# Optimization experiments

Hardware: AMD Instinct MI355X
Metric: run time of the kernel (lower is better)

The kernel has to match this reference:

```python
import jax, jax.numpy as jnp
import numpy as np

B, L, D = 2, 2048, 1024
H, NL = 16, 8
DH = D // H  # 64


def setup_inputs() -> dict:
    key = jax.random.key(0)
    ks = jax.random.split(key, 16)
    s_d = 1.0 / np.sqrt(D)
    s_ff = 1.0 / np.sqrt(4 * D)
    f32 = jnp.float32
    return {
        "x": jax.random.normal(ks[0], (B, L, D), f32),
        "pe": jax.random.normal(ks[1], (L, D), f32) / 10.0,
        "wq": jax.random.normal(ks[2], (NL, D, D), f32) * s_d,
        "wk": jax.random.normal(ks[3], (NL, D, D), f32) * s_d,
        "wv": jax.random.normal(ks[4], (NL, D, D), f32) * s_d,
        "ln1_g": 1.0 + 0.02 * jax.random.normal(ks[5], (NL, D), f32),
        "ln1_b": 0.02 * jax.random.normal(ks[6], (NL, D), f32),
        "w1": jax.random.normal(ks[7], (NL, D, 4 * D), f32) * s_d,
        "b1": jax.random.normal(ks[8], (NL, 4 * D), f32) * s_d,
        "w2": jax.random.normal(ks[9], (NL, 4 * D, D), f32) * s_ff,
        "b2": jax.random.normal(ks[10], (NL, D), f32) * s_ff,
        "ln2_g": 1.0 + 0.02 * jax.random.normal(ks[11], (NL, D), f32),
        "ln2_b": 0.02 * jax.random.normal(ks[12], (NL, D), f32),
    }


def _layernorm(x, g, b, eps=1e-5):
    m = jnp.mean(x, axis=-1, keepdims=True)
    v = jnp.mean(jnp.square(x - m), axis=-1, keepdims=True)
    return (x - m) * jax.lax.rsqrt(v + eps) * g + b


def reference(x, pe, wq, wk, wv, ln1_g, ln1_b, w1, b1, w2, b2, ln2_g, ln2_b):
    Bb, T, Dd = x.shape
    h = x + pe[:T]
    causal = jnp.tril(jnp.ones((T, T), dtype=bool))  # [T,T]
    inv_sqrt_dh = np.float32(1.0 / np.sqrt(DH))

    def step(h, p):
        wq_, wk_, wv_, g1, be1, w1_, bb1, w2_, bb2, g2, be2 = p
        # QKV: [B,T,D] -> [B,H,T,DH]
        q = (h @ wq_).reshape(Bb, T, H, DH).transpose(0, 2, 1, 3)
        k = (h @ wk_).reshape(Bb, T, H, DH).transpose(0, 2, 1, 3)
        v = (h @ wv_).reshape(Bb, T, H, DH).transpose(0, 2, 1, 3)
        scores = jnp.einsum('bhqd,bhkd->bhqk', q, k)
        scores = jnp.where(causal, scores, -jnp.inf)
        attn = jax.nn.softmax(scores * inv_sqrt_dh, axis=-1)
        o = jnp.einsum('bhqk,bhkd->bhqd', attn, v)
        o = o.transpose(0, 2, 1, 3).reshape(Bb, T, Dd)
        h = _layernorm(h + o, g1, be1)
        mlp = jax.nn.selu(h @ w1_ + bb1) @ w2_ + bb2
        h = _layernorm(h + mlp, g2, be2)
        return h, None

    h, _ = jax.lax.scan(step, h, (wq, wk, wv, ln1_g, ln1_b, w1, b1, w2, b2, ln2_g, ln2_b))
    return h
```

## Files before the change

kernel.cpp:

```cpp
#include <hip/hip_runtime.h>
#include <stdint.h>

typedef unsigned short u16;
typedef __bf16 bf16x8 __attribute__((ext_vector_type(8)));
typedef __bf16 bf16x4 __attribute__((ext_vector_type(4)));
typedef float f32x4 __attribute__((ext_vector_type(4)));

__device__ __forceinline__ float b2f(u16 b) {
    return __builtin_bit_cast(float, ((unsigned)b) << 16);
}
__device__ __forceinline__ u16 f2b(float f) {
    unsigned u = __builtin_bit_cast(unsigned, f);
    return (u16)((u + 0x7fffu + ((u >> 16) & 1u)) >> 16);
}
__device__ __forceinline__ void async16(const void* g, void* l) {
    __builtin_amdgcn_global_load_lds((const __attribute__((address_space(1))) void*)g,
                                     (__attribute__((address_space(3))) void*)l, 16, 0, 0);
}

__global__ __launch_bounds__(256) void add_pe_kernel(const float* __restrict__ x,
                                                     const float* __restrict__ pe,
                                                     float* __restrict__ hf,
                                                     u16* __restrict__ hb) {
    const size_t i = ((size_t)blockIdx.x * 256 + threadIdx.x) * 4;
    float4 xv = *(const float4*)(x + i);
    float4 pv = *(const float4*)(pe + (i & 2097151));
    float4 f;
    f.x = xv.x + pv.x; f.y = xv.y + pv.y; f.z = xv.z + pv.z; f.w = xv.w + pv.w;
    *(float4*)(hf + i) = f;
    ushort4 hv;
    hv.x = f2b(f.x); hv.y = f2b(f.y); hv.z = f2b(f.z); hv.w = f2b(f.w);
    *(ushort4*)(hb + i) = hv;
}

__global__ __launch_bounds__(256) void transpose_cast_kernel(const float* __restrict__ src,
                                                             u16* __restrict__ dst,
                                                             int srcStride, int K) {
    __shared__ __align__(16) u16 tile[64 * 72];
    const int n0 = blockIdx.x * 64, k0 = blockIdx.y * 64;
    const int t = threadIdx.x;
    const int r = t >> 3, c8 = (t & 7) * 8;
#pragma unroll
    for (int ph = 0; ph < 2; ph++) {
        const int rr = r + ph * 32;
        const float* s = src + (size_t)(k0 + rr) * srcStride + n0 + c8;
        float4 a = *(const float4*)s;
        float4 b = *(const float4*)(s + 4);
        u16* tr = tile + rr * 72 + c8;
        tr[0] = f2b(a.x); tr[1] = f2b(a.y); tr[2] = f2b(a.z); tr[3] = f2b(a.w);
        tr[4] = f2b(b.x); tr[5] = f2b(b.y); tr[6] = f2b(b.z); tr[7] = f2b(b.w);
    }
    __syncthreads();
#pragma unroll
    for (int ph = 0; ph < 2; ph++) {
        const int rr = r + ph * 32;
        union { float4 f; u16 u[8]; } ov;
#pragma unroll
        for (int j = 0; j < 8; j++) ov.u[j] = tile[(c8 + j) * 72 + rr];
        *(float4*)(dst + (size_t)(n0 + rr) * K + k0 + c8) = ov.f;
    }
}

__global__ __launch_bounds__(256) void transpose_qkv_kernel(const float* __restrict__ wq,
                                                            const float* __restrict__ wk,
                                                            const float* __restrict__ wv,
                                                            u16* __restrict__ dst) {
    __shared__ __align__(16) u16 tile[64 * 72];
    const float* src = (blockIdx.z == 0) ? wq : (blockIdx.z == 1) ? wk : wv;
    u16* d = dst + (size_t)blockIdx.z * 1048576;
    const int n0 = blockIdx.x * 64, k0 = blockIdx.y * 64;
    const int t = threadIdx.x;
    const int r = t >> 3, c8 = (t & 7) * 8;
#pragma unroll
    for (int ph = 0; ph < 2; ph++) {
        const int rr = r + ph * 32;
        const float* s = src + (size_t)(k0 + rr) * 1024 + n0 + c8;
        float4 a = *(const float4*)s;
        float4 b = *(const float4*)(s + 4);
        u16* tr = tile + rr * 72 + c8;
        tr[0] = f2b(a.x); tr[1] = f2b(a.y); tr[2] = f2b(a.z); tr[3] = f2b(a.w);
        tr[4] = f2b(b.x); tr[5] = f2b(b.y); tr[6] = f2b(b.z); tr[7] = f2b(b.w);
    }
    __syncthreads();
#pragma unroll
    for (int ph = 0; ph < 2; ph++) {
        const int rr = r + ph * 32;
        union { float4 f; u16 u[8]; } ov;
#pragma unroll
        for (int j = 0; j < 8; j++) ov.u[j] = tile[(c8 + j) * 72 + rr];
        *(float4*)(d + (size_t)(n0 + rr) * 1024 + k0 + c8) = ov.f;
    }
}

__global__ __launch_bounds__(256) void transpose_v_kernel(const u16* __restrict__ src,
                                                          u16* __restrict__ dst) {
    __shared__ __align__(16) u16 tile[64 * 72];
    const int bh = blockIdx.y, t0 = blockIdx.x * 64;
    const int t = threadIdx.x;
    const int r = t >> 3, c8 = (t & 7) * 8;
    const size_t base = (size_t)bh * 131072;
#pragma unroll
    for (int ph = 0; ph < 2; ph++) {
        const int rr = r + ph * 32;
        *(float4*)(tile + rr * 72 + c8) = *(const float4*)(src + base + (size_t)(t0 + rr) * 64 + c8);
    }
    __syncthreads();
#pragma unroll
    for (int ph = 0; ph < 2; ph++) {
        const int rr = r + ph * 32;
        union { float4 f; u16 u[8]; } ov;
#pragma unroll
        for (int j = 0; j < 8; j++) ov.u[j] = tile[(c8 + j) * 72 + rr];
        *(float4*)(dst + base + (size_t)rr * 2048 + t0 + c8) = ov.f;
    }
}

template <int MODE, int MTILES>
__global__ __launch_bounds__(256, 2) void gemm_kernel(const u16* __restrict__ A,
                                                      const u16* __restrict__ BT,
                                                      const float* __restrict__ bias,
                                                      void* __restrict__ O0, void* __restrict__ O1,
                                                      void* __restrict__ O2, int N, int K) {
    __shared__ __align__(16) u16 As[MTILES * 32 * 32];
    __shared__ __align__(16) u16 Bs[128 * 32];
    const int tid = threadIdx.x;
    const int lane = tid & 63, w = tid >> 6, quad = lane >> 4, l15 = lane & 15;
    const int m0 = blockIdx.y * (MTILES * 32), n0 = blockIdx.x * 128;
    const int wm = w >> 1, wn = w & 1;

    f32x4 acc[MTILES][4] = {};

    const int srow = tid >> 2, scol = (tid & 3) * 8;
    const u16* Ag = A + (size_t)(m0 + srow) * K + scol;
    const u16* Bg = BT + (size_t)(n0 + srow) * K + scol;
    u16* Asd = As + tid * 8;
    u16* Bsd = Bs + tid * 8;
    const size_t half = (size_t)64 * K;

    for (int k0 = 0; k0 < K; k0 += 32) {
        __syncthreads();
#pragma unroll
        for (int i = 0; i < MTILES / 2; i++) async16(Ag + k0 + i * half, Asd + i * 2048);
        async16(Bg + k0, Bsd);
        async16(Bg + k0 + half, Bsd + 2048);
        __syncthreads();
        bf16x8 af[MTILES], bfr[4];
#pragma unroll
        for (int mt = 0; mt < MTILES; mt++)
            af[mt] = *(const bf16x8*)(As + (wm * (MTILES * 16) + mt * 16 + l15) * 32 + quad * 8);
#pragma unroll
        for (int nt = 0; nt < 4; nt++)
            bfr[nt] = *(const bf16x8*)(Bs + (wn * 64 + nt * 16 + l15) * 32 + quad * 8);
#pragma unroll
        for (int mt = 0; mt < MTILES; mt++)
#pragma unroll
            for (int nt = 0; nt < 4; nt++)
                acc[mt][nt] = __builtin_amdgcn_mfma_f32_16x16x32_bf16(af[mt], bfr[nt], acc[mt][nt], 0, 0, 0);
    }

#pragma unroll
    for (int nt = 0; nt < 4; nt++) {
        const int col = n0 + wn * 64 + nt * 16 + l15;
        float bv = 0.f;
        if (MODE == 1 || MODE == 2) bv = bias[col];
#pragma unroll
        for (int mt = 0; mt < MTILES; mt++) {
#pragma unroll
            for (int r = 0; r < 4; r++) {
                const int row = m0 + wm * (MTILES * 16) + mt * 16 + quad * 4 + r;
                float val = acc[mt][nt][r];
                if (MODE == 1) {
                    val += bv;
                    const float s = 1.0507009873554805f, a = 1.6732632423543772f;
                    val = val > 0.f ? s * val : s * a * (__expf(val) - 1.f);
                    ((u16*)O0)[(size_t)row * N + col] = f2b(val);
                } else if (MODE == 2) {
                    ((float*)O0)[(size_t)row * N + col] = val + bv;
                } else {
                    ((float*)O0)[(size_t)row * N + col] += val;
                }
            }
        }
    }
}

#define G_SYNC1()                                          \
    __builtin_amdgcn_sched_barrier(0);                     \
    __builtin_amdgcn_s_barrier();                          \
    asm volatile("s_waitcnt lgkmcnt(0)" ::: "memory");     \
    __builtin_amdgcn_sched_barrier(0);                     \
    __builtin_amdgcn_s_setprio(1)
#define G_SYNC2()                                          \
    __builtin_amdgcn_s_setprio(0);                         \
    __builtin_amdgcn_sched_barrier(0);                     \
    __builtin_amdgcn_s_barrier()

template <int MODE, int NT>
__global__ __launch_bounds__(512) void gemm256_kernel(const u16* __restrict__ A,
                                                      const u16* __restrict__ BT,
                                                      const float* __restrict__ bias,
                                                      void* __restrict__ O0, void* __restrict__ O1,
                                                      void* __restrict__ O2, int N) {
    constexpr int K = NT * 64;
    __shared__ __align__(16) u16 lds[65536];
    const int tid = threadIdx.x;
    const int lane = tid & 63, w = tid >> 6, quad = lane >> 4, l15 = lane & 15;
    const int wm = w >> 2, wn = w & 3;
    const int m0 = blockIdx.y * 256, n0 = blockIdx.x * 256;

    f32x4 acc[8][4] = {};

    const int srow = tid >> 2;
    const int slog = (tid & 3) ^ ((tid >> 3) & 3);
    const u16* pA = A + (size_t)(m0 + srow) * K + slog * 8;
    const u16* pB = BT + (size_t)(n0 + srow) * K + slog * 8;
    u16* const ldst = lds + tid * 8;

    const int swz = (quad ^ ((l15 >> 1) & 3)) * 8;
    const int aro = (wm * 128 + l15) * 32 + swz;
    const int bro = 16384 + (wn * 64 + l15) * 32 + swz;

    auto stA = [&](int tt, int kh) {
        u16* d = ldst + ((tt & 1) << 15) + (kh << 13);
        const u16* s = pA + tt * 64 + kh * 32;
        async16(s, d);
        async16(s + (size_t)128 * K, d + 4096);
    };
    auto stB = [&](int tt, int kh) {
        u16* d = ldst + ((tt & 1) << 15) + 16384 + (kh << 13);
        const u16* s = pB + tt * 64 + kh * 32;
        async16(s, d);
        async16(s + (size_t)128 * K, d + 4096);
    };

    stB(0, 0); stB(0, 1); stA(0, 0); stA(0, 1);
    stB(1, 0); stB(1, 1); stA(1, 0);
    asm volatile("s_waitcnt vmcnt(6)" ::: "memory");
    __builtin_amdgcn_s_barrier();

#pragma unroll 2
    for (int t = 0; t < NT; ++t) {
        const int boff = (t & 1) << 15;
        bf16x8 a[4], bk0[4], bk1[4];
#pragma unroll
        for (int i = 0; i < 4; i++) a[i] = *(const bf16x8*)(lds + boff + aro + i * 512);
#pragma unroll
        for (int i = 0; i < 4; i++) bk0[i] = *(const bf16x8*)(lds + boff + bro + i * 512);
        if (t + 1 < NT) stA(t + 1, 1);
        G_SYNC1();
#pragma unroll
        for (int mt = 0; mt < 4; mt++)
#pragma unroll
            for (int nt = 0; nt < 4; nt++)
                acc[mt][nt] = __builtin_amdgcn_mfma_f32_16x16x32_bf16(a[mt], bk0[nt], acc[mt][nt], 0, 0, 0);
        G_SYNC2();
#pragma unroll
        for (int i = 0; i < 4; i++) a[i] = *(const bf16x8*)(lds + boff + 8192 + aro + i * 512);
#pragma unroll
        for (int i = 0; i < 4; i++) bk1[i] = *(const bf16x8*)(lds + boff + 8192 + bro + i * 512);
        if (t + 2 < NT) stB(t + 2, 0);
        G_SYNC1();
#pragma unroll
        for (int mt = 0; mt < 4; mt++)
#pragma unroll
            for (int nt = 0; nt < 4; nt++)
                acc[mt][nt] = __builtin_amdgcn_mfma_f32_16x16x32_bf16(a[mt], bk1[nt], acc[mt][nt], 0, 0, 0);
        G_SYNC2();
#pragma unroll
        for (int i = 0; i < 4; i++) a[i] = *(const bf16x8*)(lds + boff + aro + 2048 + i * 512);
        if (t + 2 < NT) stB(t + 2, 1);
        G_SYNC1();
#pragma unroll
        for (int mt = 0; mt < 4; mt++)
#pragma unroll
            for (int nt = 0; nt < 4; nt++)
                acc[4 + mt][nt] = __builtin_amdgcn_mfma_f32_16x16x32_bf16(a[mt], bk0[nt], acc[4 + mt][nt], 0, 0, 0);
        G_SYNC2();
#pragma unroll
        for (int i = 0; i < 4; i++) a[i] = *(const bf16x8*)(lds + boff + 8192 + aro + 2048 + i * 512);
        if (t + 2 < NT) stA(t + 2, 0);
        G_SYNC1();
#pragma unroll
        for (int mt = 0; mt < 4; mt++)
#pragma unroll
            for (int nt = 0; nt < 4; nt++)
                acc[4 + mt][nt] = __builtin_amdgcn_mfma_f32_16x16x32_bf16(a[mt], bk1[nt], acc[4 + mt][nt], 0, 0, 0);
        __builtin_amdgcn_s_setprio(0);
        __builtin_amdgcn_sched_barrier(0);
        if (t < NT - 2) {
            asm volatile("s_waitcnt vmcnt(6)" ::: "memory");
        } else if (t == NT - 2) {
            asm volatile("s_waitcnt vmcnt(0)" ::: "memory");
        }
        __builtin_amdgcn_sched_barrier(0);
        __builtin_amdgcn_s_barrier();
    }

#pragma unroll
    for (int nt = 0; nt < 4; nt++) {
        const int col = n0 + wn * 64 + nt * 16 + l15;
        float bv = 0.f;
        if (MODE == 1 || MODE == 2) bv = bias[col];
#pragma unroll
        for (int am = 0; am < 8; am++) {
#pragma unroll
            for (int r = 0; r < 4; r++) {
                const int row = m0 + wm * 128 + am * 16 + quad * 4 + r;
                float val = acc[am][nt][r];
                if (MODE == 0) {
                    const int mat = col >> 10, cc = col & 1023;
                    const int head = cc >> 6, dh = cc & 63;
                    const int b = row >> 11, tt = row & 2047;
                    if (mat == 0) val *= 0.18033688f;
                    u16* dst = (mat == 0) ? (u16*)O0 : (mat == 1) ? (u16*)O1 : (u16*)O2;
                    dst[(((size_t)(b * 16 + head)) * 2048 + tt) * 64 + dh] = f2b(val);
                } else if (MODE == 1) {
                    val += bv;
                    const float s = 1.0507009873554805f, aa = 1.6732632423543772f;
                    val = val > 0.f ? s * val : s * aa * (__expf(val) - 1.f);
                    ((u16*)O0)[(size_t)row * N + col] = f2b(val);
                } else if (MODE == 2) {
                    ((float*)O0)[(size_t)row * N + col] = val + bv;
                }
            }
        }
    }
}

__global__ __launch_bounds__(256) void attn_kernel(const u16* __restrict__ q,
                                                   const u16* __restrict__ k,
                                                   const u16* __restrict__ vT,
                                                   u16* __restrict__ o) {
    __shared__ __align__(16) u16 Kt[64 * 72];
    __shared__ __align__(16) u16 Vt[64 * 72];
    __shared__ __align__(16) u16 Pt[4][32 * 72];
    const int tid = threadIdx.x, lane = tid & 63, w = tid >> 6, quad = lane >> 4, l15 = lane & 15;
    const int bh = blockIdx.x;
    const int qt = 15 - blockIdx.y;
    const size_t base = (size_t)bh * 131072;
    const int wrow0 = qt * 128 + w * 32;

    bf16x8 qf[2][2];
#pragma unroll
    for (int nt = 0; nt < 2; nt++)
#pragma unroll
        for (int ks = 0; ks < 2; ks++)
            qf[nt][ks] = *(const bf16x8*)(q + base + (size_t)(wrow0 + nt * 16 + l15) * 64 + ks * 32 + quad * 8);

    float m_[2], l_[2];
    m_[0] = m_[1] = -1e30f;
    l_[0] = l_[1] = 0.f;
    f32x4 oacc[2][4] = {};

    const int ktmax = (qt + 1) * 2;
    const int srow = tid >> 3, sc8 = (tid & 7) * 8;

    for (int kt = 0; kt < ktmax; kt++) {
        __syncthreads();
#pragma unroll
        for (int ph = 0; ph < 2; ph++) {
            const int rr = srow + ph * 32;
            *(float4*)(Kt + rr * 72 + sc8) = *(const float4*)(k + base + (size_t)(kt * 64 + rr) * 64 + sc8);
            *(float4*)(Vt + rr * 72 + sc8) = *(const float4*)(vT + base + (size_t)rr * 2048 + kt * 64 + sc8);
        }
        __syncthreads();
        const bool act = (kt * 64 <= wrow0 + 31);
        if (act) {
            f32x4 st[4][2];
#pragma unroll
            for (int mt = 0; mt < 4; mt++) {
                bf16x8 kf0 = *(const bf16x8*)(Kt + (mt * 16 + l15) * 72 + quad * 8);
                bf16x8 kf1 = *(const bf16x8*)(Kt + (mt * 16 + l15) * 72 + 32 + quad * 8);
#pragma unroll
                for (int nt = 0; nt < 2; nt++) {
                    f32x4 z = {};
                    z = __builtin_amdgcn_mfma_f32_16x16x32_bf16(kf0, qf[nt][0], z, 0, 0, 0);
                    z = __builtin_amdgcn_mfma_f32_16x16x32_bf16(kf1, qf[nt][1], z, 0, 0, 0);
                    st[mt][nt] = z;
                }
            }
            const bool needmask = (kt * 64 + 63 > wrow0);
            float alpha[2];
#pragma unroll
            for (int nt = 0; nt < 2; nt++) {
                const int qg = wrow0 + nt * 16 + l15;
                float mx = -1e30f;
                if (needmask) {
#pragma unroll
                    for (int mt = 0; mt < 4; mt++)
#pragma unroll
                        for (int r = 0; r < 4; r++) {
                            const int kg = kt * 64 + mt * 16 + quad * 4 + r;
                            float s = (kg <= qg) ? st[mt][nt][r] : -1e30f;
                            st[mt][nt][r] = s;
                            mx = fmaxf(mx, s);
                        }
                } else {
#pragma unroll
                    for (int mt = 0; mt < 4; mt++)
#pragma unroll
                        for (int r = 0; r < 4; r++) mx = fmaxf(mx, st[mt][nt][r]);
                }
                mx = fmaxf(mx, __shfl_xor(mx, 16, 64));
                mx = fmaxf(mx, __shfl_xor(mx, 32, 64));
                const float mnew = fmaxf(m_[nt], mx);
                alpha[nt] = exp2f(m_[nt] - mnew);
                m_[nt] = mnew;
                float rs = 0.f;
#pragma unroll
                for (int mt = 0; mt < 4; mt++) {
                    float p0 = exp2f(st[mt][nt][0] - mnew);
                    float p1 = exp2f(st[mt][nt][1] - mnew);
                    float p2 = exp2f(st[mt][nt][2] - mnew);
                    float p3 = exp2f(st[mt][nt][3] - mnew);
                    rs += (p0 + p1) + (p2 + p3);
                    bf16x4 pk = {(__bf16)p0, (__bf16)p1, (__bf16)p2, (__bf16)p3};
                    *(bf16x4*)(Pt[w] + (nt * 16 + l15) * 72 + mt * 16 + quad * 4) = pk;
                }
                rs += __shfl_xor(rs, 16, 64);
                rs += __shfl_xor(rs, 32, 64);
                l_[nt] = l_[nt] * alpha[nt] + rs;
            }
            float arow[2][4];
#pragma unroll
            for (int mto = 0; mto < 2; mto++)
#pragma unroll
                for (int r = 0; r < 4; r++)
                    arow[mto][r] = __shfl(alpha[mto], quad * 4 + r, 64);
#pragma unroll
            for (int mto = 0; mto < 2; mto++)
#pragma unroll
                for (int ntv = 0; ntv < 4; ntv++)
#pragma unroll
                    for (int r = 0; r < 4; r++) oacc[mto][ntv][r] *= arow[mto][r];

            bf16x8 pf[2][2];
#pragma unroll
            for (int mto = 0; mto < 2; mto++)
#pragma unroll
                for (int ks = 0; ks < 2; ks++)
                    pf[mto][ks] = *(const bf16x8*)(Pt[w] + (mto * 16 + l15) * 72 + ks * 32 + quad * 8);
#pragma unroll
            for (int ntv = 0; ntv < 4; ntv++) {
                bf16x8 vf0 = *(const bf16x8*)(Vt + (ntv * 16 + l15) * 72 + quad * 8);
                bf16x8 vf1 = *(const bf16x8*)(Vt + (ntv * 16 + l15) * 72 + 32 + quad * 8);
#pragma unroll
                for (int mto = 0; mto < 2; mto++) {
                    oacc[mto][ntv] = __builtin_amdgcn_mfma_f32_16x16x32_bf16(pf[mto][0], vf0, oacc[mto][ntv], 0, 0, 0);
                    oacc[mto][ntv] = __builtin_amdgcn_mfma_f32_16x16x32_bf16(pf[mto][1], vf1, oacc[mto][ntv], 0, 0, 0);
                }
            }
        }
    }

    float linv[2] = {1.f / l_[0], 1.f / l_[1]};
    float rinv[2][4];
#pragma unroll
    for (int mto = 0; mto < 2; mto++)
#pragma unroll
        for (int r = 0; r < 4; r++)
            rinv[mto][r] = __shfl(linv[mto], quad * 4 + r, 64);

    const int b = bh >> 4, hh = bh & 15;
#pragma unroll
    for (int mto = 0; mto < 2; mto++)
#pragma unroll
        for (int ntv = 0; ntv < 4; ntv++)
#pragma unroll
            for (int r = 0; r < 4; r++) {
                const int trow = wrow0 + mto * 16 + quad * 4 + r;
                const int col = hh * 64 + ntv * 16 + l15;
                o[((size_t)b * 2048 + trow) * 1024 + col] = f2b(oacc[mto][ntv][r] * rinv[mto][r]);
            }
}

template <int ADD_BF16>
__global__ __launch_bounds__(256) void ln_kernel(const float* __restrict__ hin,
                                                 const void* __restrict__ addp,
                                                 const float* __restrict__ g,
                                                 const float* __restrict__ bt,
                                                 float* __restrict__ hf_out,
                                                 u16* __restrict__ hb_out) {
    const int w = threadIdx.x >> 6, lane = threadIdx.x & 63;
    const size_t row = (size_t)blockIdx.x * 4 + w;
    const float4* hr = (const float4*)(hin + row * 1024);
    float4 xv[4];
    float s = 0.f, s2 = 0.f;
#pragma unroll
    for (int j = 0; j < 4; j++) {
        const int idx = lane + 64 * j;
        float4 a = hr[idx];
        float4 b;
        if (ADD_BF16) {
            ushort4 av = ((const ushort4*)addp)[row * 256 + idx];
            b.x = b2f(av.x); b.y = b2f(av.y); b.z = b2f(av.z); b.w = b2f(av.w);
        } else {
            b = ((const float4*)addp)[row * 256 + idx];
        }
        float4 x;
        x.x = a.x + b.x; x.y = a.y + b.y; x.z = a.z + b.z; x.w = a.w + b.w;
        xv[j] = x;
        s += x.x + x.y + x.z + x.w;
        s2 += x.x * x.x + x.y * x.y + x.z * x.z + x.w * x.w;
    }
#pragma unroll
    for (int mm = 1; mm < 64; mm <<= 1) { s += __shfl_xor(s, mm, 64); s2 += __shfl_xor(s2, mm, 64); }
    const float mean = s * (1.f / 1024.f);
    const float var = s2 * (1.f / 1024.f) - mean * mean;
    const float rstd = rsqrtf(var + 1e-5f);
    float4* of = (float4*)(hf_out + row * 1024);
    ushort4* ob = (ushort4*)(hb_out + row * 1024);
    const float4* gv = (const float4*)g;
    const float4* bv = (const float4*)bt;
#pragma unroll
    for (int j = 0; j < 4; j++) {
        const int idx = lane + 64 * j;
        float4 gg = gv[idx], bb = bv[idx];
        float4 x = xv[j], y;
        y.x = (x.x - mean) * rstd * gg.x + bb.x;
        y.y = (x.y - mean) * rstd * gg.y + bb.y;
        y.z = (x.z - mean) * rstd * gg.z + bb.z;
        y.w = (x.w - mean) * rstd * gg.w + bb.w;
        of[idx] = y;
        ushort4 oo;
        oo.x = f2b(y.x); oo.y = f2b(y.y); oo.z = f2b(y.z); oo.w = f2b(y.w);
        ob[idx] = oo;
    }
}

extern "C" void kernel_launch(void* const* d_in, const int* in_sizes, int n_in,
                              void* d_out, int out_size, void* d_ws, size_t ws_size,
                              hipStream_t stream) {
    const float* x   = (const float*)d_in[0];
    const float* pe  = (const float*)d_in[1];
    const float* wq  = (const float*)d_in[2];
    const float* wk  = (const float*)d_in[3];
    const float* wv  = (const float*)d_in[4];
    const float* l1g = (const float*)d_in[5];
    const float* l1b = (const float*)d_in[6];
    const float* w1  = (const float*)d_in[7];
    const float* b1  = (const float*)d_in[8];
    const float* w2  = (const float*)d_in[9];
    const float* b2  = (const float*)d_in[10];
    const float* l2g = (const float*)d_in[11];
    const float* l2b = (const float*)d_in[12];

    char* ws = (char*)d_ws;
    float* hf   = (float*)(ws);
    u16* hb     = (u16*)(ws + 16777216);
    u16* qb     = (u16*)(ws + 25165824);
    u16* kb     = (u16*)(ws + 33554432);
    u16* vb     = (u16*)(ws + 41943040);
    u16* vbt    = (u16*)(ws + 50331648);
    u16* ob     = (u16*)(ws + 41943040);
    u16* wqkvT  = (u16*)(ws + 58720256);
    u16* w1T    = (u16*)(ws + 65011712);
    u16* w2T    = (u16*)(ws + 73400320);
    u16* ub     = (u16*)(ws + 81788928);
    float* mb   = (float*)(ws + 115343360);

    add_pe_kernel<<<4096, 256, 0, stream>>>(x, pe, hf, hb);

    for (int l = 0; l < 8; l++) {
        transpose_qkv_kernel<<<dim3(16, 16, 3), 256, 0, stream>>>(
            wq + (size_t)l * 1048576, wk + (size_t)l * 1048576, wv + (size_t)l * 1048576, wqkvT);
        gemm256_kernel<0, 16><<<dim3(12, 16), 512, 0, stream>>>(hb, wqkvT, nullptr, qb, kb, vb, 3072);
        transpose_v_kernel<<<dim3(32, 32), 256, 0, stream>>>(vb, vbt);
        attn_kernel<<<dim3(32, 16), 256, 0, stream>>>(qb, kb, vbt, ob);
        ln_kernel<1><<<1024, 256, 0, stream>>>(hf, ob, l1g + l * 1024, l1b + l * 1024, hf, hb);
        transpose_cast_kernel<<<dim3(64, 16), 256, 0, stream>>>(w1 + (size_t)l * 4194304, w1T, 4096, 1024);
        gemm256_kernel<1, 16><<<dim3(16, 16), 512, 0, stream>>>(hb, w1T, b1 + l * 4096, ub, nullptr, nullptr, 4096);
        transpose_cast_kernel<<<dim3(16, 64), 256, 0, stream>>>(w2 + (size_t)l * 4194304, w2T, 1024, 4096);
        gemm_kernel<2, 2><<<dim3(8, 64), 256, 0, stream>>>(ub, w2T, b2 + l * 1024, mb, nullptr, nullptr, 1024, 4096);
        const bool last = (l == 7);
        ln_kernel<0><<<1024, 256, 0, stream>>>(hf, mb, l2g + l * 1024, l2b + l * 1024,
                                               last ? (float*)d_out : hf, hb);
    }
}
```

Measured before the change: 2.290 ms.

## Batch weight transposes, split-K FFN2 with 256 tiles, double-buffer attention K/V

```diff
diff --git a/kernel.cpp b/kernel.cpp
--- a/kernel.cpp
+++ b/kernel.cpp
@@ -33,10 +33,13 @@
     *(ushort4*)(hb + i) = hv;
 }
 
-__global__ __launch_bounds__(256) void transpose_cast_kernel(const float* __restrict__ src,
-                                                             u16* __restrict__ dst,
-                                                             int srcStride, int K) {
+__global__ __launch_bounds__(256) void transpose_cast_kernel(const float* __restrict__ src0,
+                                                             u16* __restrict__ dst0,
+                                                             int srcStride, int K,
+                                                             int srcLayer, int dstLayer) {
     __shared__ __align__(16) u16 tile[64 * 72];
+    const float* src = src0 + (size_t)blockIdx.z * srcLayer;
+    u16* dst = dst0 + (size_t)blockIdx.z * dstLayer;
     const int n0 = blockIdx.x * 64, k0 = blockIdx.y * 64;
     const int t = threadIdx.x;
     const int r = t >> 3, c8 = (t & 7) * 8;
@@ -66,8 +69,10 @@
                                                             const float* __restrict__ wv,
                                                             u16* __restrict__ dst) {
     __shared__ __align__(16) u16 tile[64 * 72];
-    const float* src = (blockIdx.z == 0) ? wq : (blockIdx.z == 1) ? wk : wv;
-    u16* d = dst + (size_t)blockIdx.z * 1048576;
+    const int zz = blockIdx.z;
+    const int l = zz / 3, mat = zz - l * 3;
+    const float* src = ((mat == 0) ? wq : (mat == 1) ? wk : wv) + (size_t)l * 1048576;
+    u16* d = dst + (size_t)l * 3145728 + (size_t)mat * 1048576;
     const int n0 = blockIdx.x * 64, k0 = blockIdx.y * 64;
     const int t = threadIdx.x;
     const int r = t >> 3, c8 = (t & 7) * 8;
@@ -112,75 +117,6 @@
 #pragma unroll
         for (int j = 0; j < 8; j++) ov.u[j] = tile[(c8 + j) * 72 + rr];
         *(float4*)(dst + base + (size_t)rr * 2048 + t0 + c8) = ov.f;
-    }
-}
-
-template <int MODE, int MTILES>
-__global__ __launch_bounds__(256, 2) void gemm_kernel(const u16* __restrict__ A,
-                                                      const u16* __restrict__ BT,
-                                                      const float* __restrict__ bias,
-                                                      void* __restrict__ O0, void* __restrict__ O1,
-                                                      void* __restrict__ O2, int N, int K) {
-    __shared__ __align__(16) u16 As[MTILES * 32 * 32];
-    __shared__ __align__(16) u16 Bs[128 * 32];
-    const int tid = threadIdx.x;
-    const int lane = tid & 63, w = tid >> 6, quad = lane >> 4, l15 = lane & 15;
-    const int m0 = blockIdx.y * (MTILES * 32), n0 = blockIdx.x * 128;
-    const int wm = w >> 1, wn = w & 1;
-
-    f32x4 acc[MTILES][4] = {};
-
-    const int srow = tid >> 2, scol = (tid & 3) * 8;
-    const u16* Ag = A + (size_t)(m0 + srow) * K + scol;
-    const u16* Bg = BT + (size_t)(n0 + srow) * K + scol;
-    u16* Asd = As + tid * 8;
-    u16* Bsd = Bs + tid * 8;
-    const size_t half = (size_t)64 * K;
-
-    for (int k0 = 0; k0 < K; k0 += 32) {
-        __syncthreads();
-#pragma unroll
-        for (int i = 0; i < MTILES / 2; i++) async16(Ag + k0 + i * half, Asd + i * 2048);
-        async16(Bg + k0, Bsd);
-        async16(Bg + k0 + half, Bsd + 2048);
-        __syncthreads();
-        bf16x8 af[MTILES], bfr[4];
-#pragma unroll
-        for (int mt = 0; mt < MTILES; mt++)
-            af[mt] = *(const bf16x8*)(As + (wm * (MTILES * 16) + mt * 16 + l15) * 32 + quad * 8);
-#pragma unroll
-        for (int nt = 0; nt < 4; nt++)
-            bfr[nt] = *(const bf16x8*)(Bs + (wn * 64 + nt * 16 + l15) * 32 + quad * 8);
-#pragma unroll
-        for (int mt = 0; mt < MTILES; mt++)
-#pragma unroll
-            for (int nt = 0; nt < 4; nt++)
-                acc[mt][nt] = __builtin_amdgcn_mfma_f32_16x16x32_bf16(af[mt], bfr[nt], acc[mt][nt], 0, 0, 0);
-    }
-
-#pragma unroll
-    for (int nt = 0; nt < 4; nt++) {
-        const int col = n0 + wn * 64 + nt * 16 + l15;
-        float bv = 0.f;
-        if (MODE == 1 || MODE == 2) bv = bias[col];
-#pragma unroll
-        for (int mt = 0; mt < MTILES; mt++) {
-#pragma unroll
-            for (int r = 0; r < 4; r++) {
-                const int row = m0 + wm * (MTILES * 16) + mt * 16 + quad * 4 + r;
-                float val = acc[mt][nt][r];
-                if (MODE == 1) {
-                    val += bv;
-                    const float s = 1.0507009873554805f, a = 1.6732632423543772f;
-                    val = val > 0.f ? s * val : s * a * (__expf(val) - 1.f);
-                    ((u16*)O0)[(size_t)row * N + col] = f2b(val);
-                } else if (MODE == 2) {
-                    ((float*)O0)[(size_t)row * N + col] = val + bv;
-                } else {
-                    ((float*)O0)[(size_t)row * N + col] += val;
-                }
-            }
-        }
     }
 }
 
@@ -200,20 +136,20 @@
                                                       const u16* __restrict__ BT,
                                                       const float* __restrict__ bias,
                                                       void* __restrict__ O0, void* __restrict__ O1,
-                                                      void* __restrict__ O2, int N) {
-    constexpr int K = NT * 64;
+                                                      void* __restrict__ O2, int N, int Kstride) {
     __shared__ __align__(16) u16 lds[65536];
     const int tid = threadIdx.x;
     const int lane = tid & 63, w = tid >> 6, quad = lane >> 4, l15 = lane & 15;
     const int wm = w >> 2, wn = w & 3;
     const int m0 = blockIdx.y * 256, n0 = blockIdx.x * 256;
+    const size_t koff = (size_t)blockIdx.z * (NT * 64);
 
     f32x4 acc[8][4] = {};
 
     const int srow = tid >> 2;
     const int slog = (tid & 3) ^ ((tid >> 3) & 3);
-    const u16* pA = A + (size_t)(m0 + srow) * K + slog * 8;
-    const u16* pB = BT + (size_t)(n0 + srow) * K + slog * 8;
+    const u16* pA = A + (size_t)(m0 + srow) * Kstride + koff + slog * 8;
+    const u16* pB = BT + (size_t)(n0 + srow) * Kstride + koff + slog * 8;
     u16* const ldst = lds + tid * 8;
 
     const int swz = (quad ^ ((l15 >> 1) & 3)) * 8;
@@ -224,13 +160,13 @@
         u16* d = ldst + ((tt & 1) << 15) + (kh << 13);
         const u16* s = pA + tt * 64 + kh * 32;
         async16(s, d);
-        async16(s + (size_t)128 * K, d + 4096);
+        async16(s + (size_t)128 * Kstride, d + 4096);
     };
     auto stB = [&](int tt, int kh) {
         u16* d = ldst + ((tt & 1) << 15) + 16384 + (kh << 13);
         const u16* s = pB + tt * 64 + kh * 32;
         async16(s, d);
-        async16(s + (size_t)128 * K, d + 4096);
+        async16(s + (size_t)128 * Kstride, d + 4096);
     };
 
     stB(0, 0); stB(0, 1); stA(0, 0); stA(0, 1);
@@ -300,7 +236,7 @@
     for (int nt = 0; nt < 4; nt++) {
         const int col = n0 + wn * 64 + nt * 16 + l15;
         float bv = 0.f;
-        if (MODE == 1 || MODE == 2) bv = bias[col];
+        if (MODE == 1) bv = bias[col];
 #pragma unroll
         for (int am = 0; am < 8; am++) {
 #pragma unroll
@@ -319,8 +255,8 @@
                     const float s = 1.0507009873554805f, aa = 1.6732632423543772f;
                     val = val > 0.f ? s * val : s * aa * (__expf(val) - 1.f);
                     ((u16*)O0)[(size_t)row * N + col] = f2b(val);
-                } else if (MODE == 2) {
-                    ((float*)O0)[(size_t)row * N + col] = val + bv;
+                } else if (MODE == 4) {
+                    ((float*)O0)[((size_t)blockIdx.z * 4096 + row) * N + col] = val;
                 }
             }
         }
@@ -331,8 +267,8 @@
                                                    const u16* __restrict__ k,
                                                    const u16* __restrict__ vT,
                                                    u16* __restrict__ o) {
-    __shared__ __align__(16) u16 Kt[64 * 72];
-    __shared__ __align__(16) u16 Vt[64 * 72];
+    __shared__ __align__(16) u16 Kt[2][4096];
+    __shared__ __align__(16) u16 Vt[2][4096];
     __shared__ __align__(16) u16 Pt[4][32 * 72];
     const int tid = threadIdx.x, lane = tid & 63, w = tid >> 6, quad = lane >> 4, l15 = lane & 15;
     const int bh = blockIdx.x;
@@ -340,6 +276,23 @@
     const size_t base = (size_t)bh * 131072;
     const int wrow0 = qt * 128 + w * 32;
 
+    const int r0 = tid >> 3, s0 = (tid & 7) ^ (r0 & 7);
+    const int r1 = (tid + 256) >> 3, s1 = (tid & 7) ^ (r1 & 7);
+    const u16* kg0 = k + base + r0 * 64 + s0 * 8;
+    const u16* kg1 = k + base + r1 * 64 + s1 * 8;
+    const u16* vg0 = vT + base + (size_t)r0 * 2048 + s0 * 8;
+    const u16* vg1 = vT + base + (size_t)r1 * 2048 + s1 * 8;
+
+    auto stage = [&](int kt, int b) {
+        async16(kg0 + kt * 4096, &Kt[b][tid * 8]);
+        async16(kg1 + kt * 4096, &Kt[b][tid * 8 + 2048]);
+        async16(vg0 + (size_t)kt * 64, &Vt[b][tid * 8]);
+        async16(vg1 + (size_t)kt * 64, &Vt[b][tid * 8 + 2048]);
+    };
+
+    const int sA = (quad ^ (l15 & 7)) * 8;
+    const int sB = sA ^ 32;
+
     bf16x8 qf[2][2];
 #pragma unroll
     for (int nt = 0; nt < 2; nt++)
@@ -353,24 +306,31 @@
     f32x4 oacc[2][4] = {};
 
     const int ktmax = (qt + 1) * 2;
-    const int srow = tid >> 3, sc8 = (tid & 7) * 8;
+    stage(0, 0);
 
     for (int kt = 0; kt < ktmax; kt++) {
-        __syncthreads();
-#pragma unroll
-        for (int ph = 0; ph < 2; ph++) {
-            const int rr = srow + ph * 32;
-            *(float4*)(Kt + rr * 72 + sc8) = *(const float4*)(k + base + (size_t)(kt * 64 + rr) * 64 + sc8);
-            *(float4*)(Vt + rr * 72 + sc8) = *(const float4*)(vT + base + (size_t)rr * 2048 + kt * 64 + sc8);
+        const int cur = kt & 1;
+        if (kt + 1 < ktmax) {
+            stage(kt + 1, cur ^ 1);
+            __builtin_amdgcn_sched_barrier(0);
+            asm volatile("s_waitcnt vmcnt(4)" ::: "memory");
+        } else {
+            __builtin_amdgcn_sched_barrier(0);
+            asm volatile("s_waitcnt vmcnt(0)" ::: "memory");
         }
-        __syncthreads();
+        __builtin_amdgcn_sched_barrier(0);
+        __builtin_amdgcn_s_barrier();
+        __builtin_amdgcn_sched_barrier(0);
+        const u16* Kb = Kt[cur];
+        const u16* Vb = Vt[cur];
         const bool act = (kt * 64 <= wrow0 + 31);
         if (act) {
             f32x4 st[4][2];
+            __builtin_amdgcn_s_setprio(1);
 #pragma unroll
             for (int mt = 0; mt < 4; mt++) {
-                bf16x8 kf0 = *(const bf16x8*)(Kt + (mt * 16 + l15) * 72 + quad * 8);
-                bf16x8 kf1 = *(const bf16x8*)(Kt + (mt * 16 + l15) * 72 + 32 + quad * 8);
+                bf16x8 kf0 = *(const bf16x8*)(Kb + (mt * 16 + l15) * 64 + sA);
+                bf16x8 kf1 = *(const bf16x8*)(Kb + (mt * 16 + l15) * 64 + sB);
 #pragma unroll
                 for (int nt = 0; nt < 2; nt++) {
                     f32x4 z = {};
@@ -379,6 +339,7 @@
                     st[mt][nt] = z;
                 }
             }
+            __builtin_amdgcn_s_setprio(0);
             const bool needmask = (kt * 64 + 63 > wrow0);
             float alpha[2];
 #pragma unroll
@@ -440,17 +401,22 @@
 #pragma unroll
                 for (int ks = 0; ks < 2; ks++)
                     pf[mto][ks] = *(const bf16x8*)(Pt[w] + (mto * 16 + l15) * 72 + ks * 32 + quad * 8);
+            __builtin_amdgcn_s_setprio(1);
 #pragma unroll
             for (int ntv = 0; ntv < 4; ntv++) {
-                bf16x8 vf0 = *(const bf16x8*)(Vt + (ntv * 16 + l15) * 72 + quad * 8);
-                bf16x8 vf1 = *(const bf16x8*)(Vt + (ntv * 16 + l15) * 72 + 32 + quad * 8);
+                bf16x8 vf0 = *(const bf16x8*)(Vb + (ntv * 16 + l15) * 64 + sA);
+                bf16x8 vf1 = *(const bf16x8*)(Vb + (ntv * 16 + l15) * 64 + sB);
 #pragma unroll
                 for (int mto = 0; mto < 2; mto++) {
                     oacc[mto][ntv] = __builtin_amdgcn_mfma_f32_16x16x32_bf16(pf[mto][0], vf0, oacc[mto][ntv], 0, 0, 0);
                     oacc[mto][ntv] = __builtin_amdgcn_mfma_f32_16x16x32_bf16(pf[mto][1], vf1, oacc[mto][ntv], 0, 0, 0);
                 }
             }
+            __builtin_amdgcn_s_setprio(0);
         }
+        __builtin_amdgcn_sched_barrier(0);
+        __builtin_amdgcn_s_barrier();
+        __builtin_amdgcn_sched_barrier(0);
     }
 
     float linv[2] = {1.f / l_[0], 1.f / l_[1]};
@@ -474,11 +440,12 @@
             }
 }
 
-template <int ADD_BF16>
+template <int AM>
 __global__ __launch_bounds__(256) void ln_kernel(const float* __restrict__ hin,
                                                  const void* __restrict__ addp,
                                                  const float* __restrict__ g,
                                                  const float* __restrict__ bt,
+                                                 const float* __restrict__ bias2,
                                                  float* __restrict__ hf_out,
                                                  u16* __restrict__ hb_out) {
     const int w = threadIdx.x >> 6, lane = threadIdx.x & 63;
@@ -491,11 +458,21 @@
         const int idx = lane + 64 * j;
         float4 a = hr[idx];
         float4 b;
-        if (ADD_BF16) {
+        if (AM == 1) {
             ushort4 av = ((const ushort4*)addp)[row * 256 + idx];
             b.x = b2f(av.x); b.y = b2f(av.y); b.z = b2f(av.z); b.w = b2f(av.w);
         } else {
-            b = ((const float4*)addp)[row * 256 + idx];
+            const float4* pp = (const float4*)addp;
+            const size_t po = row * 256 + idx;
+            float4 p0 = pp[po];
+            float4 p1 = pp[po + 1048576];
+            float4 p2 = pp[po + 2097152];
+            float4 p3 = pp[po + 3145728];
+            float4 bb2 = ((const float4*)bias2)[idx];
+            b.x = (p0.x + p1.x) + (p2.x + p3.x) + bb2.x;
+            b.y = (p0.y + p1.y) + (p2.y + p3.y) + bb2.y;
+            b.z = (p0.z + p1.z) + (p2.z + p3.z) + bb2.z;
+            b.w = (p0.w + p1.w) + (p2.w + p3.w) + bb2.w;
         }
         float4 x;
         x.x = a.x + b.x; x.y = a.y + b.y; x.z = a.z + b.z; x.w = a.w + b.w;
@@ -551,29 +528,31 @@
     u16* qb     = (u16*)(ws + 25165824);
     u16* kb     = (u16*)(ws + 33554432);
     u16* vb     = (u16*)(ws + 41943040);
+    u16* ob     = (u16*)(ws + 41943040);
     u16* vbt    = (u16*)(ws + 50331648);
-    u16* ob     = (u16*)(ws + 41943040);
-    u16* wqkvT  = (u16*)(ws + 58720256);
-    u16* w1T    = (u16*)(ws + 65011712);
-    u16* w2T    = (u16*)(ws + 73400320);
-    u16* ub     = (u16*)(ws + 81788928);
-    float* mb   = (float*)(ws + 115343360);
+    u16* ub     = (u16*)(ws + 58720256);
+    float* mb   = (float*)(ws + 92274688);
+    u16* wqkvT  = (u16*)(ws + 159383552);
+    u16* w1T    = (u16*)(ws + 209715200);
+    u16* w2T    = (u16*)(ws + 276824064);
 
     add_pe_kernel<<<4096, 256, 0, stream>>>(x, pe, hf, hb);
+    transpose_qkv_kernel<<<dim3(16, 16, 24), 256, 0, stream>>>(wq, wk, wv, wqkvT);
+    transpose_cast_kernel<<<dim3(64, 16, 8), 256, 0, stream>>>(w1, w1T, 4096, 1024, 4194304, 4194304);
+    transpose_cast_kernel<<<dim3(16, 64, 8), 256, 0, stream>>>(w2, w2T, 1024, 4096, 4194304, 4194304);
 
     for (int l = 0; l < 8; l++) {
-        transpose_qkv_kernel<<<dim3(16, 16, 3), 256, 0, stream>>>(
-            wq + (size_t)l * 1048576, wk + (size_t)l * 1048576, wv + (size_t)l * 1048576, wqkvT);
-        gemm256_kernel<0, 16><<<dim3(12, 16), 512, 0, stream>>>(hb, wqkvT, nullptr, qb, kb, vb, 3072);
+        gemm256_kernel<0, 16><<<dim3(12, 16), 512, 0, stream>>>(
+            hb, wqkvT + (size_t)l * 3145728, nullptr, qb, kb, vb, 3072, 1024);
         transpose_v_kernel<<<dim3(32, 32), 256, 0, stream>>>(vb, vbt);
         attn_kernel<<<dim3(32, 16), 256, 0, stream>>>(qb, kb, vbt, ob);
-        ln_kernel<1><<<1024, 256, 0, stream>>>(hf, ob, l1g + l * 1024, l1b + l * 1024, hf, hb);
-        transpose_cast_kernel<<<dim3(64, 16), 256, 0, stream>>>(w1 + (size_t)l * 4194304, w1T, 4096, 1024);
-        gemm256_kernel<1, 16><<<dim3(16, 16), 512, 0, stream>>>(hb, w1T, b1 + l * 4096, ub, nullptr, nullptr, 4096);
-        transpose_cast_kernel<<<dim3(16, 64), 256, 0, stream>>>(w2 + (size_t)l * 4194304, w2T, 1024, 4096);
-        gemm_kernel<2, 2><<<dim3(8, 64), 256, 0, stream>>>(ub, w2T, b2 + l * 1024, mb, nullptr, nullptr, 1024, 4096);
+        ln_kernel<1><<<1024, 256, 0, stream>>>(hf, ob, l1g + l * 1024, l1b + l * 1024, nullptr, hf, hb);
+        gemm256_kernel<1, 16><<<dim3(16, 16), 512, 0, stream>>>(
+            hb, w1T + (size_t)l * 4194304, b1 + l * 4096, ub, nullptr, nullptr, 4096, 1024);
+        gemm256_kernel<4, 16><<<dim3(4, 16, 4), 512, 0, stream>>>(
+            ub, w2T + (size_t)l * 4194304, nullptr, mb, nullptr, nullptr, 1024, 4096);
         const bool last = (l == 7);
-        ln_kernel<0><<<1024, 256, 0, stream>>>(hf, mb, l2g + l * 1024, l2b + l * 1024,
-                                               last ? (float*)d_out : hf, hb);
-    }
-}
+        ln_kernel<2><<<1024, 256, 0, stream>>>(hf, mb, l2g + l * 1024, l2b + l * 1024,
+                                               b2 + l * 1024, last ? (float*)d_out : hf, hb);
+    }
+}
```

Measured after the change: 2.190 ms. 4.4% less time.
